# Performance work log

Hardware: AMD Instinct MI355X
Metric: run time of the kernel (lower is better)

## Reference

```python
import jax, jax.numpy as jnp
import numpy as np

B, S, C, H, E, K = 8, 512, 768, 12, 8, 2
MLP_H = int(C * 4.0)
HD = C // H
ROUTER_REG = 0.01
LN_EPS = 1e-5


def setup_inputs() -> dict:
    key = jax.random.key(0)
    ks = jax.random.split(key, 8)

    def w(k, shape, fan_in):
        return (jax.random.normal(k, shape, dtype=jnp.float32) / np.sqrt(fan_in)).astype(jnp.float32)

    return {
        "x": jax.random.normal(ks[0], (B, S, C), dtype=jnp.float32),
        "expert_tokens": w(ks[1], (E, C), C),
        "ln1_g": jnp.ones((E, C), jnp.float32),
        "ln1_b": jnp.zeros((E, C), jnp.float32),
        "qkv_w": w(ks[2], (E, C, 3 * C), C),
        "qkv_b": jnp.zeros((E, 3 * C), jnp.float32),
        "proj_w": w(ks[3], (E, C, C), C),
        "proj_b": jnp.zeros((E, C), jnp.float32),
        "ln2_g": jnp.ones((E, C), jnp.float32),
        "ln2_b": jnp.zeros((E, C), jnp.float32),
        "fc1_w": w(ks[4], (E, C, MLP_H), C),
        "fc1_b": jnp.zeros((E, MLP_H), jnp.float32),
        "fc2_w": w(ks[5], (E, MLP_H, C), MLP_H),
        "fc2_b": jnp.zeros((E, C), jnp.float32),
    }


def _layernorm(x, g, b):
    mu = jnp.mean(x, axis=-1, keepdims=True)
    var = jnp.mean(jnp.square(x - mu), axis=-1, keepdims=True)
    return (x - mu) * jax.lax.rsqrt(var + LN_EPS) * g + b


def _block(x, p):
    # One transformer Block (pre-LN attention + MLP), params for a single expert.
    ln1_g, ln1_b, qkv_w, qkv_b, proj_w, proj_b, ln2_g, ln2_b, fc1_w, fc1_b, fc2_w, fc2_b = p
    h = _layernorm(x, ln1_g, ln1_b)
    qkv = (h @ qkv_w + qkv_b).reshape(B, S, 3, H, HD)
    q, k, v = qkv[:, :, 0], qkv[:, :, 1], qkv[:, :, 2]  # [B,S,H,HD]
    # NOTE: original code MULTIPLIES by sqrt(head_dim) (scale = head_dim**0.5).
    scale = jnp.float32(np.sqrt(HD))
    attn = jax.nn.softmax(jnp.einsum('bqhd,bkhd->bhqk', q, k) * scale, axis=-1)
    o = jnp.einsum('bhqk,bkhd->bqhd', attn, v).reshape(B, S, C)
    x = x + (o @ proj_w + proj_b)
    h2 = _layernorm(x, ln2_g, ln2_b)
    x = x + (jax.nn.gelu(h2 @ fc1_w + fc1_b, approximate=False) @ fc2_w + fc2_b)
    return x


def reference(x, expert_tokens, ln1_g, ln1_b, qkv_w, qkv_b, proj_w, proj_b,
              ln2_g, ln2_b, fc1_w, fc1_b, fc2_w, fc2_b):
    # Router
    router_logits = jnp.einsum('bsc,nc->bsn', x, expert_tokens) / jnp.float32(np.sqrt(C))
    router_probs = jax.nn.softmax(router_logits, axis=-1)
    top_k_probs, top_k_idx = jax.lax.top_k(router_probs, K)  # [B,S,K]
    top_k_probs = top_k_probs / jnp.sum(top_k_probs, axis=-1, keepdims=True)

    # Dense all-expert compute (sequential over experts to bound memory)
    params = (ln1_g, ln1_b, qkv_w, qkv_b, proj_w, proj_b, ln2_g, ln2_b,
              fc1_w, fc1_b, fc2_w, fc2_b)
    expert_out = jax.lax.map(lambda p: _block(x, p), params)  # [E,B,S,C]
    expert_out = jnp.transpose(expert_out, (1, 2, 0, 3))       # [B,S,E,C]

    # Top-k gather and weighted combine
    sel = jnp.take_along_axis(expert_out, top_k_idx[..., None], axis=2)  # [B,S,K,C]
    combine = jnp.sum(sel * top_k_probs[..., None], axis=2)
    out = x + combine

    # Load-balance auxiliary loss
    counts = jnp.sum(jax.nn.one_hot(top_k_idx, E, dtype=jnp.float32), axis=(0, 1, 2))
    f_i = counts / jnp.float32(B * S * K)
    P_i = jnp.mean(router_probs, axis=(0, 1))
    balance_loss = E * jnp.sum(f_i * P_i) + ROUTER_REG * jnp.linalg.norm(expert_tokens)
    return out, balance_loss
```

## Files before the change

### kernel.cpp

```cpp
#include <hip/hip_runtime.h>
#include <hip/hip_bf16.h>

#define BB 8
#define SS 512
#define CC 768
#define HH 12
#define HD 64
#define EE 8
#define KK 2
#define MLPH 3072
#define NT (BB*SS)
#define NOUT (NT*CC)

#define SLOTB      68059136ull
#define SLOT_U16   34029568ull
#define SLOT_F32   17014784ull

typedef unsigned int u32;
typedef unsigned short u16;
typedef __attribute__((ext_vector_type(8))) short short8;
typedef __attribute__((ext_vector_type(4))) float f32x4;

__device__ __forceinline__ u16 f2bf(float f) {
    u32 u = __builtin_bit_cast(u32, f);
    u32 r = (u + 0x7fffu + ((u >> 16) & 1u)) >> 16;
    return (u16)r;
}
__device__ __forceinline__ float bf2f(u16 h) {
    u32 u = ((u32)h) << 16;
    return __builtin_bit_cast(float, u);
}
__device__ __forceinline__ void gl_lds16(const void* g, void* l) {
    __builtin_amdgcn_global_load_lds(
        (const __attribute__((address_space(1))) u32*)g,
        (__attribute__((address_space(3))) u32*)l, 16, 0, 0);
}
__device__ __forceinline__ void swz_rc(int bid, int& bm, int& bn) {
    int xcd = bid & 7, off = bid >> 3;
    bm = (xcd * 4 + (off & 3)) * 128;
    bn = (off >> 2) * 128;
}

__device__ __forceinline__ void stage128x64(const u16* __restrict__ G, size_t ldg,
                                            u16* s, int tid)
{
    int wid = tid >> 6, lane = tid & 63;
#pragma unroll
    for (int it = 0; it < 4; ++it) {
        int cb = it * 256 + wid * 64;
        int c = cb + lane;
        int row = c >> 3;
        int ch = (c & 7) ^ (row & 7);
        gl_lds16(G + (size_t)row * ldg + ch * 8, s + cb * 8);
    }
}
__device__ __forceinline__ short8 frag64(const u16* s, int row, int kc, int lb) {
    int ch = (kc * 4 + lb) ^ (row & 7);
    return *(const short8*)(s + row * 64 + ch * 8);
}

__device__ __forceinline__ void stg_dp(const u16* __restrict__ A, const u16* __restrict__ B,
                                       int ldk, u16* sA, u16* sB, int t, int tid)
{
    int wid = tid >> 6, lane = tid & 63;
#pragma unroll
    for (int rd = 0; rd < 2; rd++) {
        int cb = rd * 256 + wid * 64;
        int c = cb + lane;
        gl_lds16(A + (size_t)(c >> 2) * ldk + t * 32 + (c & 3) * 8, sA + cb * 8);
    }
#pragma unroll
    for (int rd = 0; rd < 2; rd++) {
        int cb = rd * 256 + wid * 64;
        int c = cb + lane;
        gl_lds16(B + (size_t)(c >> 2) * ldk + t * 32 + (c & 3) * 8, sB + cb * 8);
    }
}

__global__ __launch_bounds__(256) void router_kernel(const float* __restrict__ x,
    const float* __restrict__ et, float* __restrict__ W, float* __restrict__ stats)
{
    __shared__ float etl[EE * CC];
    __shared__ float pred[4][2 * EE];
    int tid = threadIdx.x;
    for (int i = tid; i < EE * CC; i += 256) etl[i] = et[i];
    __syncthreads();
    int wid = tid >> 6, lane = tid & 63;
    float psum[EE] = {}, csum[EE] = {};
    for (int i = 0; i < 2; i++) {
        int t = blockIdx.x * 8 + wid * 2 + i;
        const float* xr = x + (size_t)t * CC;
        float acc[EE] = {};
        for (int c = lane; c < CC; c += 64) {
            float xv = xr[c];
#pragma unroll
            for (int e = 0; e < EE; e++) acc[e] += xv * etl[e * CC + c];
        }
#pragma unroll
        for (int e = 0; e < EE; e++)
            for (int off = 1; off < 64; off <<= 1) acc[e] += __shfl_xor(acc[e], off, 64);
        if (lane == 0) {
            const float inv = 0.03608439182435161f;
            float l[EE], m = -1e30f;
#pragma unroll
            for (int e = 0; e < EE; e++) { l[e] = acc[e] * inv; m = fmaxf(m, l[e]); }
            float p[EE], sum = 0.f;
#pragma unroll
            for (int e = 0; e < EE; e++) { p[e] = __expf(l[e] - m); sum += p[e]; }
            int i1 = 0;
#pragma unroll
            for (int e = 1; e < EE; e++) if (p[e] > p[i1]) i1 = e;
            int i2 = -1;
#pragma unroll
            for (int e = 0; e < EE; e++) if (e != i1 && (i2 < 0 || p[e] > p[i2])) i2 = e;
            float wn = p[i1] + p[i2];
#pragma unroll
            for (int e = 0; e < EE; e++) W[t * EE + e] = 0.f;
            W[t * EE + i1] = p[i1] / wn;
            W[t * EE + i2] = p[i2] / wn;
#pragma unroll
            for (int e = 0; e < EE; e++) psum[e] += p[e] / sum;
            csum[i1] += 1.f; csum[i2] += 1.f;
        }
    }
    if (lane == 0) {
#pragma unroll
        for (int e = 0; e < EE; e++) { pred[wid][e] = psum[e]; pred[wid][EE + e] = csum[e]; }
    }
    __syncthreads();
    if (tid < 2 * EE) {
        float s = pred[0][tid] + pred[1][tid] + pred[2][tid] + pred[3][tid];
        atomicAdd(&stats[tid], s);
    }
}

template<int MODE>
__global__ __launch_bounds__(256) void ln_kernel(const float* __restrict__ x, size_t xslot,
    u16* __restrict__ out_hi, u16* __restrict__ out_lo, size_t oslot)
{
    int t = blockIdx.x;
    int eb = blockIdx.y;
    const float* xr = x + (size_t)eb * xslot + (size_t)t * CC;
    __shared__ float red[256];
    int tid = threadIdx.x;
    float v[3];
    float s = 0.f;
#pragma unroll
    for (int i = 0; i < 3; i++) { v[i] = xr[tid + i * 256]; s += v[i]; }
    red[tid] = s; __syncthreads();
    for (int off = 128; off > 0; off >>= 1) { if (tid < off) red[tid] += red[tid + off]; __syncthreads(); }
    float mu = red[0] / (float)CC;
    __syncthreads();
    float s2 = 0.f;
#pragma unroll
    for (int i = 0; i < 3; i++) { float d = v[i] - mu; s2 += d * d; }
    red[tid] = s2; __syncthreads();
    for (int off = 128; off > 0; off >>= 1) { if (tid < off) red[tid] += red[tid + off]; __syncthreads(); }
    float var = red[0] / (float)CC;
    float sc = rsqrtf(var + 1e-5f);
#pragma unroll
    for (int i = 0; i < 3; i++) {
        int c = tid + i * 256;
        float val = (v[i] - mu) * sc;
        u16 hi = f2bf(val);
        out_hi[(size_t)eb * oslot + (size_t)t * CC + c] = hi;
        if (MODE) out_lo[(size_t)eb * oslot + (size_t)t * CC + c] = f2bf(val - bf2f(hi));
    }
}

__global__ __launch_bounds__(256) void prep_expert(
    const float* __restrict__ qkv_w0, const float* __restrict__ qkv_b0,
    const float* __restrict__ proj_w0,
    const float* __restrict__ fc1_w0, const float* __restrict__ fc1_b0,
    const float* __restrict__ fc2_w0,
    const float* __restrict__ g1_0, const float* __restrict__ b1_0,
    const float* __restrict__ g2_0, const float* __restrict__ b2_0,
    u16* __restrict__ qkvTh, u16* __restrict__ qkvTl,
    u16* __restrict__ projT, u16* __restrict__ fc1T, u16* __restrict__ fc2T,
    float* __restrict__ biasq, float* __restrict__ biasf1, int ebase)
{
    __shared__ float tile[32][33];
    __shared__ float bsh[CC];
    __shared__ float redg[256];
    int bid = blockIdx.x;
    int eb = blockIdx.y;
    int ge = ebase + eb;
    int tid = threadIdx.x;
    const float* qkv_w = qkv_w0 + (size_t)ge * CC * 3 * CC;
    const float* qkv_b = qkv_b0 + (size_t)ge * 3 * CC;
    const float* proj_w = proj_w0 + (size_t)ge * CC * CC;
    const float* fc1_w = fc1_w0 + (size_t)ge * CC * MLPH;
    const float* fc1_b = fc1_b0 + (size_t)ge * MLPH;
    const float* fc2_w = fc2_w0 + (size_t)ge * MLPH * CC;
    const float* g1 = g1_0 + (size_t)ge * CC;
    const float* b1 = b1_0 + (size_t)ge * CC;
    const float* g2 = g2_0 + (size_t)ge * CC;
    const float* b2 = b2_0 + (size_t)ge * CC;

    if (bid < 6912) {
        const float* src; const float* scale = nullptr;
        u16 *dh, *dl = nullptr; int N, Kd, n0, k0;
        if (bid < 1728) {
            src = qkv_w; scale = g1;
            dh = qkvTh + (size_t)eb * SLOT_U16; dl = qkvTl + (size_t)eb * SLOT_U16;
            N = 2304; Kd = 768; n0 = (bid % 72) * 32; k0 = (bid / 72) * 32;
        } else if (bid < 2304) {
            int i = bid - 1728;
            src = proj_w; dh = projT + (size_t)eb * SLOT_U16; N = 768; Kd = 768;
            n0 = (i % 24) * 32; k0 = (i / 24) * 32;
        } else if (bid < 4608) {
            int i = bid - 2304;
            src = fc1_w; scale = g2; dh = fc1T + (size_t)eb * SLOT_U16; N = 3072; Kd = 768;
            n0 = (i % 96) * 32; k0 = (i / 96) * 32;
        } else {
            int i = bid - 4608;
            src = fc2_w; dh = fc2T + (size_t)eb * SLOT_U16; N = 768; Kd = 3072;
            n0 = (i % 24) * 32; k0 = (i / 24) * 32;
        }
        int tx = tid & 31, ty = tid >> 5;
#pragma unroll
        for (int i = 0; i < 32; i += 8) {
            float v = src[(size_t)(k0 + ty + i) * N + n0 + tx];
            if (scale) v *= scale[k0 + ty + i];
            tile[ty + i][tx] = v;
        }
        __syncthreads();
#pragma unroll
        for (int i = 0; i < 32; i += 8) {
            float v = tile[tx][ty + i];
            u16 hi = f2bf(v);
            dh[(size_t)(n0 + ty + i) * Kd + k0 + tx] = hi;
            if (dl) dl[(size_t)(n0 + ty + i) * Kd + k0 + tx] = f2bf(v - bf2f(hi));
        }
    } else {
        const float* bv; const float* wsrc; const float* badd;
        float* dst; int N, n0;
        if (bid < 6984) { bv = b1; wsrc = qkv_w; badd = qkv_b; dst = biasq + (size_t)eb * SLOT_F32; N = 2304; n0 = (bid - 6912) * 32; }
        else            { bv = b2; wsrc = fc1_w; badd = fc1_b; dst = biasf1 + (size_t)eb * SLOT_F32; N = MLPH; n0 = (bid - 6984) * 32; }
        for (int i = tid; i < CC; i += 256) bsh[i] = bv[i];
        __syncthreads();
        int g = tid & 31, l8 = tid >> 5;
        int n = n0 + g;
        float acc = 0.f;
        for (int k = l8; k < CC; k += 8) acc += bsh[k] * wsrc[(size_t)k * N + n];
        redg[tid] = acc; __syncthreads();
        if (tid < 32) {
            float sum = 0.f;
#pragma unroll
            for (int i = 0; i < 8; i++) sum += redg[tid + i * 32];
            dst[n0 + tid] = sum + badd[n0 + tid];
        }
    }
}

__global__ __launch_bounds__(256) void gemm_qkv_bk64(
    const u16* __restrict__ Ah, const u16* __restrict__ Al,
    const u16* __restrict__ Bh0, const u16* __restrict__ Bl0,
    const float* __restrict__ biasq0, u16* __restrict__ qk_hi0,
    u16* __restrict__ vraw0)
{
    __shared__ __align__(16) u16 sAh[128 * 64], sAl[128 * 64];
    __shared__ __align__(16) u16 sBh[128 * 64], sBl[128 * 64];
    int tid = threadIdx.x;
    int eb = blockIdx.y;
    int bm, bn;
    swz_rc(blockIdx.x, bm, bn);
    bool qk_tile = (bn < 1536);
    int wid = tid >> 6, lane = tid & 63;
    int wr = wid >> 1, wc = wid & 1;
    int la = lane & 15, lb = lane >> 4;
    const u16* Bh = Bh0 + (size_t)eb * SLOT_U16;
    const u16* Bl = Bl0 + (size_t)eb * SLOT_U16;
    const float* bias = biasq0 + (size_t)eb * SLOT_F32;
    u16* qk_hi = qk_hi0 + (size_t)eb * SLOT_U16;
    u16* vraw = vraw0 + (size_t)eb * SLOT_U16;

    f32x4 acc[4][4];
#pragma unroll
    for (int i = 0; i < 4; i++)
#pragma unroll
        for (int j = 0; j < 4; j++) acc[i][j] = (f32x4){0.f, 0.f, 0.f, 0.f};

    const u16* Abh = Ah + (size_t)bm * CC;
    const u16* Abl = Al + (size_t)bm * CC;
    const u16* Bbh = Bh + (size_t)bn * CC;
    const u16* Bbl = Bl + (size_t)bn * CC;
    for (int k0 = 0; k0 < CC; k0 += 64) {
        stage128x64(Abh + k0, CC, sAh, tid);
        stage128x64(Bbh + k0, CC, sBh, tid);
        if (qk_tile) {
            stage128x64(Abl + k0, CC, sAl, tid);
            stage128x64(Bbl + k0, CC, sBl, tid);
        }
        __syncthreads();
        if (qk_tile) {
#pragma unroll
            for (int kc = 0; kc < 2; kc++) {
                short8 avh[4], avl[4], bvh[4], bvl[4];
#pragma unroll
                for (int i = 0; i < 4; i++) {
                    int row = wr * 64 + i * 16 + la;
                    avh[i] = frag64(sAh, row, kc, lb);
                    avl[i] = frag64(sAl, row, kc, lb);
                }
#pragma unroll
                for (int j = 0; j < 4; j++) {
                    int row = wc * 64 + j * 16 + la;
                    bvh[j] = frag64(sBh, row, kc, lb);
                    bvl[j] = frag64(sBl, row, kc, lb);
                }
#pragma unroll
                for (int i = 0; i < 4; i++)
#pragma unroll
                    for (int j = 0; j < 4; j++) {
                        acc[i][j] = __builtin_amdgcn_mfma_f32_16x16x32_bf16(avh[i], bvh[j], acc[i][j], 0, 0, 0);
                        acc[i][j] = __builtin_amdgcn_mfma_f32_16x16x32_bf16(avh[i], bvl[j], acc[i][j], 0, 0, 0);
                        acc[i][j] = __builtin_amdgcn_mfma_f32_16x16x32_bf16(avl[i], bvh[j], acc[i][j], 0, 0, 0);
                    }
            }
        } else {
#pragma unroll
            for (int kc = 0; kc < 2; kc++) {
                short8 avh[4], bvh[4];
#pragma unroll
                for (int i = 0; i < 4; i++) avh[i] = frag64(sAh, wr * 64 + i * 16 + la, kc, lb);
#pragma unroll
                for (int j = 0; j < 4; j++) bvh[j] = frag64(sBh, wc * 64 + j * 16 + la, kc, lb);
#pragma unroll
                for (int i = 0; i < 4; i++)
#pragma unroll
                    for (int j = 0; j < 4; j++)
                        acc[i][j] = __builtin_amdgcn_mfma_f32_16x16x32_bf16(avh[i], bvh[j], acc[i][j], 0, 0, 0);
            }
        }
        __syncthreads();
    }
#pragma unroll
    for (int i = 0; i < 4; i++) {
#pragma unroll
        for (int j = 0; j < 4; j++) {
            int gn = bn + wc * 64 + j * 16 + la;
            float bsv = bias[gn];
#pragma unroll
            for (int r = 0; r < 4; r++) {
                int gm = bm + wr * 64 + i * 16 + lb * 4 + r;
                float v = acc[i][j][r] + bsv;
                if (qk_tile) {
                    qk_hi[(size_t)gm * 1536 + gn] = f2bf(v);
                } else {
                    vraw[(size_t)gm * CC + (gn - 1536)] = f2bf(v);
                }
            }
        }
    }
}

__global__ __launch_bounds__(256) void vtrans(const u16* __restrict__ vraw0,
    u16* __restrict__ vt0)
{
    __shared__ u16 tile[64][65];
    int st = blockIdx.x;
    int h = blockIdx.y;
    int z = blockIdx.z;
    int b = z & (BB - 1), eb = z >> 3;
    const u16* vraw = vraw0 + (size_t)eb * SLOT_U16;
    u16* vt = vt0 + (size_t)eb * SLOT_U16;
    int tid = threadIdx.x;
    int row = tid >> 3, ch = tid & 7;
#pragma unroll
    for (int it = 0; it < 2; it++) {
        int s = it * 32 + row;
        const u16* src = vraw + (size_t)(b * SS + st * 64 + s) * CC + h * HD + ch * 8;
        short8 v = *(const short8*)src;
#pragma unroll
        for (int k = 0; k < 8; k++) tile[s][ch * 8 + k] = (u16)v[k];
    }
    __syncthreads();
#pragma unroll
    for (int it = 0; it < 2; it++) {
        int d = it * 32 + row;
        u16* dst = vt + ((size_t)((b * HH + h) * HD + d)) * SS + st * 64 + ch * 8;
        short8 v;
#pragma unroll
        for (int k = 0; k < 8; k++) v[k] = (short)tile[ch * 8 + k][d];
        *(short8*)dst = v;
    }
}

template<int EPI>
__device__ __forceinline__ void gemm_dp_body(
    const u16* __restrict__ Ab, const u16* __restrict__ Bb, int Kdim,
    const float* __restrict__ biasp, const float* __restrict__ resp,
    const float* __restrict__ Wt, int ge, const float* __restrict__ xinit,
    void* __restrict__ Cout, int N, int bm, int bn)
{
    __shared__ __align__(16) u16 sA[3][128 * 32];
    __shared__ __align__(16) u16 sB[3][128 * 32];
    int tid = threadIdx.x;
    int wid = tid >> 6, lane = tid & 63;
    int wr = wid >> 1, wc = wid & 1;
    int la = lane & 15, lb = lane >> 4;
    int NTILE = Kdim / 32;

    f32x4 acc[4][4];
#pragma unroll
    for (int i = 0; i < 4; i++)
#pragma unroll
        for (int j = 0; j < 4; j++) acc[i][j] = (f32x4){0.f, 0.f, 0.f, 0.f};

    stg_dp(Ab, Bb, Kdim, sA[0], sB[0], 0, tid);
    stg_dp(Ab, Bb, Kdim, sA[1], sB[1], 1, tid);

    for (int t = 0; t < NTILE; t++) {
        if (t < NTILE - 1) asm volatile("s_waitcnt vmcnt(4)" ::: "memory");
        else               asm volatile("s_waitcnt vmcnt(0)" ::: "memory");
        __builtin_amdgcn_s_barrier();
        asm volatile("" ::: "memory");

        const u16* cA = &sA[t % 3][0];
        const u16* cB = &sB[t % 3][0];
        __builtin_amdgcn_s_setprio(1);
        short8 bv[4];
#pragma unroll
        for (int j = 0; j < 4; j++)
            bv[j] = *(const short8*)(cB + ((size_t)(wc * 64 + j * 16 + la) * 4 + lb) * 8);
#pragma unroll
        for (int i = 0; i < 4; i++) {
            short8 av = *(const short8*)(cA + ((size_t)(wr * 64 + i * 16 + la) * 4 + lb) * 8);
#pragma unroll
            for (int j = 0; j < 4; j++)
                acc[i][j] = __builtin_amdgcn_mfma_f32_16x16x32_bf16(av, bv[j], acc[i][j], 0, 0, 0);
        }
        __builtin_amdgcn_s_setprio(0);

        if (t + 2 < NTILE) stg_dp(Ab, Bb, Kdim, sA[(t + 2) % 3], sB[(t + 2) % 3], t + 2, tid);
    }

#pragma unroll
    for (int i = 0; i < 4; i++) {
#pragma unroll
        for (int j = 0; j < 4; j++) {
            int gn = bn + wc * 64 + j * 16 + la;
            float bsv = biasp[gn];
#pragma unroll
            for (int r = 0; r < 4; r++) {
                int gm = bm + wr * 64 + i * 16 + lb * 4 + r;
                size_t idx = (size_t)gm * N + gn;
                float v = acc[i][j][r] + bsv;
                if (EPI == 1) {
                    ((float*)Cout)[idx] = resp[idx] + v;
                } else if (EPI == 2) {
                    float gel = 0.5f * v * (1.0f + erff(v * 0.70710678118654752f));
                    ((u16*)Cout)[idx] = f2bf(gel);
                } else {
                    float w = Wt[(size_t)gm * EE + ge];
                    float val = w * (v + resp[idx]);
                    if (ge == 0) val += xinit[idx];
                    atomicAdd(&((float*)Cout)[idx], val);
                }
            }
        }
    }
}

__global__ __launch_bounds__(256) void gemm_proj_dp(
    const u16* __restrict__ A0, const u16* __restrict__ BT0,
    const float* __restrict__ bias0, const float* __restrict__ x,
    float* __restrict__ C0)
{
    int eb = blockIdx.y;
    int bm, bn;
    swz_rc(blockIdx.x, bm, bn);
    gemm_dp_body<1>(A0 + (size_t)eb * SLOT_U16 + (size_t)bm * CC,
                    BT0 + (size_t)eb * SLOT_U16 + (size_t)bn * CC, CC,
                    bias0 + (size_t)eb * CC, x, nullptr, 0, nullptr,
                    C0 + (size_t)eb * SLOT_F32, CC, bm, bn);
}

__global__ __launch_bounds__(256) void gemm_fc1_dp(
    const u16* __restrict__ A0, const u16* __restrict__ BT0,
    const float* __restrict__ bias0, u16* __restrict__ C0)
{
    int eb = blockIdx.y;
    int bm, bn;
    swz_rc(blockIdx.x, bm, bn);
    gemm_dp_body<2>(A0 + (size_t)eb * SLOT_U16 + (size_t)bm * CC,
                    BT0 + (size_t)eb * SLOT_U16 + (size_t)bn * CC, CC,
                    bias0 + (size_t)eb * SLOT_F32, nullptr, nullptr, 0, nullptr,
                    C0 + (size_t)eb * SLOT_U16, MLPH, bm, bn);
}

__global__ __launch_bounds__(256) void gemm_fc2_dp(
    const u16* __restrict__ A0, const u16* __restrict__ BT0,
    const float* __restrict__ bias0, const float* __restrict__ res0,
    const float* __restrict__ Wt, int ebase, const float* __restrict__ xinit,
    float* __restrict__ Cout)
{
    int eb = blockIdx.y;
    int bm, bn;
    swz_rc(blockIdx.x, bm, bn);
    gemm_dp_body<5>(A0 + (size_t)eb * SLOT_U16 + (size_t)bm * MLPH,
                    BT0 + (size_t)eb * SLOT_U16 + (size_t)bn * MLPH, MLPH,
                    bias0 + (size_t)eb * CC, res0 + (size_t)eb * SLOT_F32,
                    Wt, ebase + eb, xinit, Cout, CC, bm, bn);
}

__global__ __launch_bounds__(256) void attn_mfma(const u16* __restrict__ qk_hi0,
    const u16* __restrict__ vt0, u16* __restrict__ o0)
{
    int q0 = blockIdx.x * 64;
    int h = blockIdx.y;
    int z = blockIdx.z;
    int b = z & (BB - 1), eb = z >> 3;
    int tid = threadIdx.x, wid = tid >> 6, lane = tid & 63;
    int la = lane & 15, lb = lane >> 4;
    __shared__ __align__(16) u16 Ksh[64 * 64];
    __shared__ __align__(16) u16 Vs[64 * 64];
    __shared__ __align__(16) u16 Ps[4][16 * 64];

    const u16* qk_hi = qk_hi0 + (size_t)eb * SLOT_U16;
    const u16* vt = vt0 + (size_t)eb * SLOT_U16;
    u16* o = o0 + (size_t)eb * SLOT_U16;

    short8 aqh[2];
    {
        size_t qoff = (size_t)(b * SS + q0 + wid * 16 + la) * 1536 + h * HD;
#pragma unroll
        for (int kc = 0; kc < 2; kc++)
            aqh[kc] = *(const short8*)(qk_hi + qoff + kc * 32 + lb * 8);
    }
    const u16* kbh = qk_hi + (size_t)(b * SS) * 1536 + CC + h * HD;
    const u16* vtbase = vt + (size_t)((b * HH + h) * HD) * SS;

    float m_r[4], l_r[4];
    f32x4 acc_o[4];
#pragma unroll
    for (int r = 0; r < 4; r++) { m_r[r] = -1e30f; l_r[r] = 0.f; }
#pragma unroll
    for (int d0 = 0; d0 < 4; d0++) acc_o[d0] = (f32x4){0.f, 0.f, 0.f, 0.f};

    for (int kt = 0; kt < SS; kt += 64) {
#pragma unroll
        for (int it = 0; it < 2; it++) {
            int base = it * 256 + wid * 64;
            int c = base + lane;
            int row = c >> 3;
            int gk = (c & 7) ^ (row & 7);
            gl_lds16(kbh + (size_t)(kt + row) * 1536 + gk * 8, Ksh + base * 8);
            gl_lds16(vtbase + (size_t)row * SS + kt + gk * 8, Vs + base * 8);
        }
        __syncthreads();

        f32x4 s4[4];
#pragma unroll
        for (int j = 0; j < 4; j++) s4[j] = (f32x4){0.f, 0.f, 0.f, 0.f};
#pragma unroll
        for (int kc = 0; kc < 2; kc++)
#pragma unroll
            for (int j = 0; j < 4; j++) {
                size_t off = (size_t)(j * 16 + la) * 64 + (((kc * 4 + lb) ^ (la & 7)) * 8);
                short8 bkh = *(const short8*)(Ksh + off);
                s4[j] = __builtin_amdgcn_mfma_f32_16x16x32_bf16(aqh[kc], bkh, s4[j], 0, 0, 0);
            }
#pragma unroll
        for (int j = 0; j < 4; j++) s4[j] = s4[j] * 8.f;

#pragma unroll
        for (int r = 0; r < 4; r++) {
            float mx = fmaxf(fmaxf(s4[0][r], s4[1][r]), fmaxf(s4[2][r], s4[3][r]));
#pragma unroll
            for (int off = 1; off < 16; off <<= 1) mx = fmaxf(mx, __shfl_xor(mx, off, 64));
            float mn = fmaxf(m_r[r], mx);
            float corr = __expf(m_r[r] - mn);
            m_r[r] = mn;
            float rs = 0.f;
#pragma unroll
            for (int j = 0; j < 4; j++) {
                float p = __expf(s4[j][r] - mn);
                s4[j][r] = p; rs += p;
            }
#pragma unroll
            for (int off = 1; off < 16; off <<= 1) rs += __shfl_xor(rs, off, 64);
            l_r[r] = l_r[r] * corr + rs;
#pragma unroll
            for (int d0 = 0; d0 < 4; d0++) acc_o[d0][r] = acc_o[d0][r] * corr;
        }
#pragma unroll
        for (int j = 0; j < 4; j++)
#pragma unroll
            for (int r = 0; r < 4; r++) {
                int row = lb * 4 + r;
                int sg = (2 * j + (la >> 3)) ^ (row & 7);
                Ps[wid][row * 64 + sg * 8 + (la & 7)] = f2bf(s4[j][r]);
            }
        short8 pa[2];
#pragma unroll
        for (int kc = 0; kc < 2; kc++)
            pa[kc] = *(const short8*)(&Ps[wid][la * 64 + (((kc * 4 + lb) ^ (la & 7)) * 8)]);
#pragma unroll
        for (int d0 = 0; d0 < 4; d0++)
#pragma unroll
            for (int kc = 0; kc < 2; kc++) {
                short8 bv = *(const short8*)(&Vs[(d0 * 16 + la) * 64 + (((kc * 4 + lb) ^ (la & 7)) * 8)]);
                acc_o[d0] = __builtin_amdgcn_mfma_f32_16x16x32_bf16(pa[kc], bv, acc_o[d0], 0, 0, 0);
            }
        __syncthreads();
    }
#pragma unroll
    for (int r = 0; r < 4; r++) {
        float invl = 1.f / l_r[r];
        int tok = b * SS + q0 + wid * 16 + lb * 4 + r;
#pragma unroll
        for (int d0 = 0; d0 < 4; d0++)
            o[(size_t)tok * CC + h * HD + d0 * 16 + la] = f2bf(acc_o[d0][r] * invl);
    }
}

__global__ __launch_bounds__(256) void loss_kernel(const float* __restrict__ et,
    const float* __restrict__ stats, float* __restrict__ out_loss)
{
    __shared__ float red[256];
    int tid = threadIdx.x;
    float s = 0.f;
    for (int i = tid; i < EE * CC; i += 256) { float v = et[i]; s += v * v; }
    red[tid] = s; __syncthreads();
    for (int off = 128; off > 0; off >>= 1) { if (tid < off) red[tid] += red[tid + off]; __syncthreads(); }
    if (tid == 0) {
        float bl = 0.f;
        for (int e = 0; e < EE; e++) {
            float f = stats[EE + e] / (float)(NT * KK);
            float P = stats[e] / (float)NT;
            bl += f * P;
        }
        *out_loss = (float)EE * bl + 0.01f * sqrtf(red[0]);
    }
}

extern "C" void kernel_launch(void* const* d_in, const int* in_sizes, int n_in,
                              void* d_out, int out_size, void* d_ws, size_t ws_size,
                              hipStream_t stream) {
    const float* x      = (const float*)d_in[0];
    const float* et     = (const float*)d_in[1];
    const float* ln1_g  = (const float*)d_in[2];
    const float* ln1_b  = (const float*)d_in[3];
    const float* qkv_w  = (const float*)d_in[4];
    const float* qkv_b  = (const float*)d_in[5];
    const float* proj_w = (const float*)d_in[6];
    const float* proj_b = (const float*)d_in[7];
    const float* ln2_g  = (const float*)d_in[8];
    const float* ln2_b  = (const float*)d_in[9];
    const float* fc1_w  = (const float*)d_in[10];
    const float* fc1_b  = (const float*)d_in[11];
    const float* fc2_w  = (const float*)d_in[12];
    const float* fc2_b  = (const float*)d_in[13];
    float* outp = (float*)d_out;
    char* base = (char*)d_ws;

    const size_t FIXED = 12714496;
    int EB = 1;
    if (ws_size >= FIXED + 8 * SLOTB) EB = 8;
    else if (ws_size >= FIXED + 4 * SLOTB) EB = 4;
    else if (ws_size >= FIXED + 2 * SLOTB) EB = 2;

    float* W      = (float*)(base);
    float* stats  = (float*)(base + 131072);
    u16*   xh_hi  = (u16*)  (base + 131584);
    u16*   xh_lo  = (u16*)  (base + 6423040);
    char* slot0 = base + FIXED;
    u16*   qkvTh  = (u16*)  (slot0);
    u16*   qkvTl  = (u16*)  (slot0 + 3538944);
    u16*   projT  = (u16*)  (slot0 + 7077888);
    u16*   fc1T   = (u16*)  (slot0 + 8257536);
    u16*   fc2T   = (u16*)  (slot0 + 12976128);
    float* biasq  = (float*)(slot0 + 17694720);
    float* biasf1 = (float*)(slot0 + 17711104);
    u16*   qk_hi  = (u16*)  (slot0 + 17727488);
    u16*   mlp1   = (u16*)  (slot0 + 17727488);
    u16*   vtb    = (u16*)  (slot0 + 42893312);
    u16*   xmhat  = (u16*)  (slot0 + 42893312);
    u16*   obf    = (u16*)  (slot0 + 49184768);
    u16*   vraw   = obf;
    float* xmid   = (float*)(slot0 + 55476224);

    hipMemsetAsync(stats, 0, 16 * sizeof(float), stream);
    hipMemsetAsync(outp, 0, (size_t)NOUT * sizeof(float), stream);

    router_kernel<<<NT / 8, 256, 0, stream>>>(x, et, W, stats);
    ln_kernel<1><<<dim3(NT, 1), 256, 0, stream>>>(x, 0, xh_hi, xh_lo, 0);

    for (int ebase = 0; ebase < EE; ebase += EB) {
        prep_expert<<<dim3(7080, EB), 256, 0, stream>>>(
            qkv_w, qkv_b, proj_w, fc1_w, fc1_b, fc2_w,
            ln1_g, ln1_b, ln2_g, ln2_b,
            qkvTh, qkvTl, projT, fc1T, fc2T, biasq, biasf1, ebase);

        gemm_qkv_bk64<<<dim3(18 * 32, EB), 256, 0, stream>>>(
            xh_hi, xh_lo, qkvTh, qkvTl, biasq, qk_hi, vraw);

        vtrans<<<dim3(SS / 64, HH, BB * EB), 256, 0, stream>>>(vraw, vtb);

        attn_mfma<<<dim3(SS / 64, HH, BB * EB), 256, 0, stream>>>(qk_hi, vtb, obf);

        gemm_proj_dp<<<dim3(6 * 32, EB), 256, 0, stream>>>(
            obf, projT, proj_b + (size_t)ebase * CC, x, xmid);

        ln_kernel<0><<<dim3(NT, EB), 256, 0, stream>>>(xmid, SLOT_F32, xmhat, nullptr, SLOT_U16);

        gemm_fc1_dp<<<dim3(24 * 32, EB), 256, 0, stream>>>(xmhat, fc1T, biasf1, mlp1);

        gemm_fc2_dp<<<dim3(6 * 32, EB), 256, 0, stream>>>(
            mlp1, fc2T, fc2_b + (size_t)ebase * CC, xmid, W, ebase, x, outp);
    }

    loss_kernel<<<1, 256, 0, stream>>>(et, stats, outp + NOUT);
}
```

Measured before the change: 1.357 ms.

## Split-K fc2 GEMM in two halves and XOR-swizzle dp GEMM LDS tiles

The fc2 GEMM (K=3072) is split into two K halves launched as twice as many blocks. Both halves atomically add into the output, and only the first half adds the bias, residual and initial x. Separately, the double-pumped GEMM LDS layout now packs two rows per 64-element line with an XOR swizzle, aiming to reduce LDS bank conflicts on fragment reads. The split raises parallelism for the low-occupancy fc2 grid at the cost of doubled atomic traffic on the output.

```diff
diff --git a/kernel.cpp b/kernel.cpp
--- a/kernel.cpp
+++ b/kernel.cpp
@@ -59,21 +59,33 @@
     return *(const short8*)(s + row * 64 + ch * 8);
 }
 
-__device__ __forceinline__ void stg_dp(const u16* __restrict__ A, const u16* __restrict__ B,
-                                       int ldk, u16* sA, u16* sB, int t, int tid)
+__device__ __forceinline__ size_t dpidx(int r, int lb) {
+    int L = r >> 1;
+    int slot = (((r & 1) << 2) | lb) ^ (L & 7);
+    return (size_t)L * 64 + slot * 8;
+}
+
+__device__ __forceinline__ void stg_dp2(const u16* __restrict__ A, const u16* __restrict__ B,
+                                        int ldk, int koff, u16* sA, u16* sB, int tid)
 {
     int wid = tid >> 6, lane = tid & 63;
 #pragma unroll
     for (int rd = 0; rd < 2; rd++) {
         int cb = rd * 256 + wid * 64;
         int c = cb + lane;
-        gl_lds16(A + (size_t)(c >> 2) * ldk + t * 32 + (c & 3) * 8, sA + cb * 8);
+        int L = c >> 3, sp = c & 7;
+        int slog = sp ^ (L & 7);
+        int row = 2 * L + (slog >> 2), ch = slog & 3;
+        gl_lds16(A + (size_t)row * ldk + koff + ch * 8, sA + (size_t)cb * 8);
     }
 #pragma unroll
     for (int rd = 0; rd < 2; rd++) {
         int cb = rd * 256 + wid * 64;
         int c = cb + lane;
-        gl_lds16(B + (size_t)(c >> 2) * ldk + t * 32 + (c & 3) * 8, sB + cb * 8);
+        int L = c >> 3, sp = c & 7;
+        int slog = sp ^ (L & 7);
+        int row = 2 * L + (slog >> 2), ch = slog & 3;
+        gl_lds16(B + (size_t)row * ldk + koff + ch * 8, sB + (size_t)cb * 8);
     }
 }
 
@@ -389,9 +401,9 @@
 
 template<int EPI>
 __device__ __forceinline__ void gemm_dp_body(
-    const u16* __restrict__ Ab, const u16* __restrict__ Bb, int Kdim,
+    const u16* __restrict__ Ab, const u16* __restrict__ Bb, int ldk, int klen,
     const float* __restrict__ biasp, const float* __restrict__ resp,
-    const float* __restrict__ Wt, int ge, const float* __restrict__ xinit,
+    const float* __restrict__ Wt, int ge, int ks, const float* __restrict__ xinit,
     void* __restrict__ Cout, int N, int bm, int bn)
 {
     __shared__ __align__(16) u16 sA[3][128 * 32];
@@ -400,7 +412,7 @@
     int wid = tid >> 6, lane = tid & 63;
     int wr = wid >> 1, wc = wid & 1;
     int la = lane & 15, lb = lane >> 4;
-    int NTILE = Kdim / 32;
+    int NTILE = klen / 32;
 
     f32x4 acc[4][4];
 #pragma unroll
@@ -408,8 +420,8 @@
 #pragma unroll
         for (int j = 0; j < 4; j++) acc[i][j] = (f32x4){0.f, 0.f, 0.f, 0.f};
 
-    stg_dp(Ab, Bb, Kdim, sA[0], sB[0], 0, tid);
-    stg_dp(Ab, Bb, Kdim, sA[1], sB[1], 1, tid);
+    stg_dp2(Ab, Bb, ldk, 0, sA[0], sB[0], tid);
+    stg_dp2(Ab, Bb, ldk, 32, sA[1], sB[1], tid);
 
     for (int t = 0; t < NTILE; t++) {
         if (t < NTILE - 1) asm volatile("s_waitcnt vmcnt(4)" ::: "memory");
@@ -423,17 +435,17 @@
         short8 bv[4];
 #pragma unroll
         for (int j = 0; j < 4; j++)
-            bv[j] = *(const short8*)(cB + ((size_t)(wc * 64 + j * 16 + la) * 4 + lb) * 8);
+            bv[j] = *(const short8*)(cB + dpidx(wc * 64 + j * 16 + la, lb));
 #pragma unroll
         for (int i = 0; i < 4; i++) {
-            short8 av = *(const short8*)(cA + ((size_t)(wr * 64 + i * 16 + la) * 4 + lb) * 8);
+            short8 av = *(const short8*)(cA + dpidx(wr * 64 + i * 16 + la, lb));
 #pragma unroll
             for (int j = 0; j < 4; j++)
                 acc[i][j] = __builtin_amdgcn_mfma_f32_16x16x32_bf16(av, bv[j], acc[i][j], 0, 0, 0);
         }
         __builtin_amdgcn_s_setprio(0);
 
-        if (t + 2 < NTILE) stg_dp(Ab, Bb, Kdim, sA[(t + 2) % 3], sB[(t + 2) % 3], t + 2, tid);
+        if (t + 2 < NTILE) stg_dp2(Ab, Bb, ldk, (t + 2) * 32, sA[(t + 2) % 3], sB[(t + 2) % 3], tid);
     }
 
 #pragma unroll
@@ -446,16 +458,22 @@
             for (int r = 0; r < 4; r++) {
                 int gm = bm + wr * 64 + i * 16 + lb * 4 + r;
                 size_t idx = (size_t)gm * N + gn;
-                float v = acc[i][j][r] + bsv;
+                float v = acc[i][j][r];
                 if (EPI == 1) {
-                    ((float*)Cout)[idx] = resp[idx] + v;
+                    ((float*)Cout)[idx] = resp[idx] + v + bsv;
                 } else if (EPI == 2) {
-                    float gel = 0.5f * v * (1.0f + erff(v * 0.70710678118654752f));
+                    float g = v + bsv;
+                    float gel = 0.5f * g * (1.0f + erff(g * 0.70710678118654752f));
                     ((u16*)Cout)[idx] = f2bf(gel);
                 } else {
                     float w = Wt[(size_t)gm * EE + ge];
-                    float val = w * (v + resp[idx]);
-                    if (ge == 0) val += xinit[idx];
+                    float val;
+                    if (ks == 0) {
+                        val = w * (v + bsv + resp[idx]);
+                        if (ge == 0) val += xinit[idx];
+                    } else {
+                        val = w * v;
+                    }
                     atomicAdd(&((float*)Cout)[idx], val);
                 }
             }
@@ -472,8 +490,8 @@
     int bm, bn;
     swz_rc(blockIdx.x, bm, bn);
     gemm_dp_body<1>(A0 + (size_t)eb * SLOT_U16 + (size_t)bm * CC,
-                    BT0 + (size_t)eb * SLOT_U16 + (size_t)bn * CC, CC,
-                    bias0 + (size_t)eb * CC, x, nullptr, 0, nullptr,
+                    BT0 + (size_t)eb * SLOT_U16 + (size_t)bn * CC, CC, CC,
+                    bias0 + (size_t)eb * CC, x, nullptr, 0, 0, nullptr,
                     C0 + (size_t)eb * SLOT_F32, CC, bm, bn);
 }
 
@@ -485,8 +503,8 @@
     int bm, bn;
     swz_rc(blockIdx.x, bm, bn);
     gemm_dp_body<2>(A0 + (size_t)eb * SLOT_U16 + (size_t)bm * CC,
-                    BT0 + (size_t)eb * SLOT_U16 + (size_t)bn * CC, CC,
-                    bias0 + (size_t)eb * SLOT_F32, nullptr, nullptr, 0, nullptr,
+                    BT0 + (size_t)eb * SLOT_U16 + (size_t)bn * CC, CC, CC,
+                    bias0 + (size_t)eb * SLOT_F32, nullptr, nullptr, 0, 0, nullptr,
                     C0 + (size_t)eb * SLOT_U16, MLPH, bm, bn);
 }
 
@@ -497,12 +515,15 @@
     float* __restrict__ Cout)
 {
     int eb = blockIdx.y;
+    int ks = blockIdx.x / 192;
+    int bid = blockIdx.x - ks * 192;
     int bm, bn;
-    swz_rc(blockIdx.x, bm, bn);
-    gemm_dp_body<5>(A0 + (size_t)eb * SLOT_U16 + (size_t)bm * MLPH,
-                    BT0 + (size_t)eb * SLOT_U16 + (size_t)bn * MLPH, MLPH,
+    swz_rc(bid, bm, bn);
+    int koff = ks * (MLPH / 2);
+    gemm_dp_body<5>(A0 + (size_t)eb * SLOT_U16 + (size_t)bm * MLPH + koff,
+                    BT0 + (size_t)eb * SLOT_U16 + (size_t)bn * MLPH + koff, MLPH, MLPH / 2,
                     bias0 + (size_t)eb * CC, res0 + (size_t)eb * SLOT_F32,
-                    Wt, ebase + eb, xinit, Cout, CC, bm, bn);
+                    Wt, ebase + eb, ks, xinit, Cout, CC, bm, bn);
 }
 
 __global__ __launch_bounds__(256) void attn_mfma(const u16* __restrict__ qk_hi0,
@@ -708,7 +729,7 @@
 
         gemm_fc1_dp<<<dim3(24 * 32, EB), 256, 0, stream>>>(xmhat, fc1T, biasf1, mlp1);
 
-        gemm_fc2_dp<<<dim3(6 * 32, EB), 256, 0, stream>>>(
+        gemm_fc2_dp<<<dim3(2 * 6 * 32, EB), 256, 0, stream>>>(
             mlp1, fc2T, fc2_b + (size_t)ebase * CC, xmid, W, ebase, x, outp);
     }
 
```

Result: slower. 1.411 ms (+4.0%).
